# Kernel tuning notes

Measured on AMD Instinct MI355X. Metric: run time of the kernel, lower is better.

The kernel has to match this reference:

```python
import jax, jax.numpy as jnp
import numpy as np

N_NODES = 50000
N_EDGES = 1600000
IN_DIM = 6
H = 64


def _sage_conv(x, src, dst, W_l, b_l, W_r, num_nodes):
    """PyG SAGEConv (aggr='mean'): out = lin_l(mean_{j in N(i)} x_j) + lin_r(x_i).
    lin_l has bias, lin_r has no bias (PyG default)."""
    # mean-aggregate neighbor features at destination nodes
    agg = jax.ops.segment_sum(x[src], dst, num_segments=num_nodes)          # [N, d]
    cnt = jax.ops.segment_sum(jnp.ones((src.shape[0],), x.dtype), dst,
                              num_segments=num_nodes)                        # [N]
    mean = agg / jnp.maximum(cnt, 1.0)[:, None]
    return mean @ W_l + b_l + x @ W_r


def setup_inputs() -> dict:
    key = jax.random.key(0)
    ks = jax.random.split(key, 8)
    x = jax.random.normal(ks[0], (N_NODES, IN_DIM), dtype=jnp.float32)
    edge_index = jax.random.randint(ks[1], (2, N_EDGES), 0, N_NODES, dtype=jnp.int64)
    # Kaiming-ish scaled params
    def lin(k, fan_in, fan_out):
        return jax.random.normal(k, (fan_in, fan_out), dtype=jnp.float32) / np.sqrt(fan_in)
    return {
        "x": x,
        "edge_index": edge_index,
        "W1_l": lin(ks[2], IN_DIM, H),
        "b1_l": jnp.zeros((H,), jnp.float32),
        "W1_r": lin(ks[3], IN_DIM, H),
        "W2_l": lin(ks[4], H, H),
        "b2_l": jnp.zeros((H,), jnp.float32),
        "W2_r": lin(ks[5], H, H),
    }


def reference(x, edge_index, W1_l, b1_l, W1_r, W2_l, b2_l, W2_r):
    src, dst = edge_index[0], edge_index[1]
    n = x.shape[0]
    z = jax.nn.relu(_sage_conv(x, src, dst, W1_l, b1_l, W1_r, n))  # [N, H]
    z = _sage_conv(z, src, dst, W2_l, b2_l, W2_r, n)               # [N, H]
    return z
```

## Files before the change

### kernel.cpp

```cpp
#include <hip/hip_runtime.h>

#define N_NODES 50000
#define N_EDGES 1600000
#define IN_DIM 6
#define H 64

#define NBUCKET 196
#define NBLK 196
#define EPB 8192
#define BCAP 9216

#define L2PAD 72

__device__ __forceinline__ float bf2f(unsigned short u) {
    return __uint_as_float(((unsigned int)u) << 16);
}
__device__ __forceinline__ unsigned short f2bf(float f) {
    unsigned int u = __float_as_uint(f);
    u += 0x7fffu + ((u >> 16) & 1u);
    return (unsigned short)(u >> 16);
}

__global__ __launch_bounds__(512) void scatter_bucketed(
        const int* __restrict__ ei,
        int* __restrict__ gcur,
        unsigned int* __restrict__ ebin,
        const float* __restrict__ W2l,
        const float* __restrict__ W2r,
        unsigned short* __restrict__ Wlt,
        unsigned short* __restrict__ Wrt,
        unsigned short* __restrict__ z) {
    int t = threadIdx.x;
    if (blockIdx.x == NBLK) {
        for (int i = t; i < H * H; i += 512) {
            int k = i >> 6, f = i & 63;
            Wlt[f * H + k] = f2bf(W2l[i]);
            Wrt[f * H + k] = f2bf(W2r[i]);
        }
        if (t < H) z[(size_t)N_NODES * H + t] = 0;
        return;
    }
    __shared__ unsigned int sedge[EPB];
    __shared__ int hist[NBUCKET];
    __shared__ int cur[NBUCKET];
    for (int i = t; i < NBUCKET; i += 512) hist[i] = 0;
    __syncthreads();
    int e0 = blockIdx.x * EPB;
    int cnt = min(EPB, N_EDGES - e0);
    const int4* s4 = (const int4*)(ei + e0);
    const int4* d4 = (const int4*)(ei + N_EDGES + e0);
    for (int k = t; k * 4 < cnt; k += 512) {
        int4 sv = s4[k];
        int4 dv = d4[k];
        sedge[k * 4 + 0] = ((unsigned)sv.x << 16) | (unsigned)dv.x;
        sedge[k * 4 + 1] = ((unsigned)sv.y << 16) | (unsigned)dv.y;
        sedge[k * 4 + 2] = ((unsigned)sv.z << 16) | (unsigned)dv.z;
        sedge[k * 4 + 3] = ((unsigned)sv.w << 16) | (unsigned)dv.w;
        atomicAdd(&hist[dv.x >> 8], 1);
        atomicAdd(&hist[dv.y >> 8], 1);
        atomicAdd(&hist[dv.z >> 8], 1);
        atomicAdd(&hist[dv.w >> 8], 1);
    }
    __syncthreads();
    for (int i = t; i < NBUCKET; i += 512)
        cur[i] = atomicAdd(&gcur[i], hist[i]);
    __syncthreads();
    for (int k = t; k * 4 < cnt; k += 512) {
#pragma unroll
        for (int j = 0; j < 4; j++) {
            unsigned int p = sedge[k * 4 + j];
            int b = (int)(p & 0xffffu) >> 8;
            int pos = atomicAdd(&cur[b], 1);
            if (pos < BCAP) ebin[(size_t)b * BCAP + pos] = p;
        }
    }
}

__global__ __launch_bounds__(1024) void bucket_layer1(
        const unsigned int* __restrict__ ebin,
        const int* __restrict__ gcur,
        const float* __restrict__ x,
        const float* __restrict__ W1l,
        const float* __restrict__ b1,
        const float* __restrict__ W1r,
        int2* __restrict__ rowpair,
        unsigned short* __restrict__ esrc,
        unsigned short* __restrict__ z) {
    __shared__ int raw[BCAP];
    __shared__ unsigned short ssrc[BCAP];
    __shared__ int sdeg[256];
    __shared__ int sstart[256];
    __shared__ int scur[256];
    __shared__ int wsum[4];
    __shared__ float sW1l[IN_DIM * H];
    __shared__ float sW1r[IN_DIM * H];
    float* smx   = (float*)raw;
    float* spart = (float*)raw + 4096;

    int t = threadIdx.x;
    int lane = t & 63, w = t >> 6;
    int b = blockIdx.x;
    int base = b << 8;
    int nn = min(256, N_NODES - base);
    int ebase = b * BCAP;
    int cnt = min(gcur[b], BCAP);

    if (t < 256) sdeg[t] = 0;
    if (t < IN_DIM * H) { sW1l[t] = W1l[t]; sW1r[t] = W1r[t]; }
    for (int i = t; i < cnt; i += 1024) raw[i] = (int)ebin[ebase + i];
    __syncthreads();
    for (int i = t; i < cnt; i += 1024) atomicAdd(&sdeg[raw[i] & 0xff], 1);
    __syncthreads();
    int v = 0, s = 0;
    if (t < 256) {
        v = sdeg[t]; s = v;
#pragma unroll
        for (int off = 1; off < 64; off <<= 1) {
            int u = __shfl_up(s, off);
            if (lane >= off) s += u;
        }
        if (lane == 63) wsum[w] = s;
    }
    __syncthreads();
    if (t < 256) {
        int woff = 0;
        for (int k = 0; k < w; k++) woff += wsum[k];
        int excl = s - v + woff;
        sstart[t] = excl;
        scur[t] = excl;
        if (t < nn) rowpair[base + t] = make_int2(ebase + excl, ebase + excl + v);
    }
    __syncthreads();
    for (int i = t; i < cnt; i += 1024) {
        int p = raw[i];
        int pos = atomicAdd(&scur[p & 0xff], 1);
        ssrc[pos] = (unsigned short)((unsigned)p >> 16);
    }
    __syncthreads();
    for (int i = t; i < cnt; i += 1024)
        esrc[ebase + i] = ssrc[i];
    for (int i = t; i < nn * IN_DIM; i += 1024) {
        int node = i / 6, k = i - node * 6;
        smx[node * 16 + 6 + k] = x[(size_t)base * IN_DIM + i];
    }

    int node = t & 255, q = t >> 8;
    float a0 = 0.f, a1 = 0.f, a2 = 0.f, a3 = 0.f, a4 = 0.f, a5 = 0.f;
    int deg = 0, st = 0;
    if (node < nn) { deg = sdeg[node]; st = sstart[node]; }
    for (int i = st + q; i < st + deg; i += 4) {
        int src = ssrc[i];
        const float2* xs = (const float2*)(x + (size_t)src * IN_DIM);
        float2 p0 = xs[0], p1 = xs[1], p2 = xs[2];
        a0 += p0.x; a1 += p0.y; a2 += p1.x;
        a3 += p1.y; a4 += p2.x; a5 += p2.y;
    }
    if (q > 0 && node < nn) {
        float* sp = &spart[(q - 1) * (256 * 6) + node * 6];
        sp[0] = a0; sp[1] = a1; sp[2] = a2; sp[3] = a3; sp[4] = a4; sp[5] = a5;
    }
    __syncthreads();
    if (q == 0 && node < nn) {
        float inv = 1.0f / fmaxf((float)deg, 1.0f);
        const float* p1p = &spart[0 * (256 * 6) + node * 6];
        const float* p2p = &spart[1 * (256 * 6) + node * 6];
        const float* p3p = &spart[2 * (256 * 6) + node * 6];
        smx[node * 16 + 0] = (a0 + p1p[0] + p2p[0] + p3p[0]) * inv;
        smx[node * 16 + 1] = (a1 + p1p[1] + p2p[1] + p3p[1]) * inv;
        smx[node * 16 + 2] = (a2 + p1p[2] + p2p[2] + p3p[2]) * inv;
        smx[node * 16 + 3] = (a3 + p1p[3] + p2p[3] + p3p[3]) * inv;
        smx[node * 16 + 4] = (a4 + p1p[4] + p2p[4] + p3p[4]) * inv;
        smx[node * 16 + 5] = (a5 + p1p[5] + p2p[5] + p3p[5]) * inv;
    }
    __syncthreads();

    int feat = t & 63, ng = t >> 6;
    float wl[IN_DIM], wr[IN_DIM];
#pragma unroll
    for (int k = 0; k < IN_DIM; k++) { wl[k] = sW1l[k * H + feat]; wr[k] = sW1r[k * H + feat]; }
    float bias = b1[feat];
    for (int nb = ng; nb < nn; nb += 16) {
        const float4* row = (const float4*)&smx[nb * 16];
        float4 r0 = row[0], r1 = row[1], r2 = row[2];
        float acc = bias;
        acc += r0.x * wl[0] + r0.y * wl[1] + r0.z * wl[2]
             + r0.w * wl[3] + r1.x * wl[4] + r1.y * wl[5];
        acc += r1.z * wr[0] + r1.w * wr[1] + r2.x * wr[2]
             + r2.y * wr[3] + r2.z * wr[4] + r2.w * wr[5];
        z[(size_t)(base + nb) * H + feat] = f2bf(fmaxf(acc, 0.0f));
    }
}

__global__ __launch_bounds__(512) void layer2_mfma(
        const unsigned short* __restrict__ zin,
        const int2* __restrict__ rowpair,
        const unsigned short* __restrict__ esrc,
        const unsigned short* __restrict__ Wlt,
        const float* __restrict__ b2,
        const unsigned short* __restrict__ Wrt,
        float* __restrict__ out) {
    typedef short bf16x8 __attribute__((ext_vector_type(8)));
    typedef float f32x4 __attribute__((ext_vector_type(4)));
    __shared__ __attribute__((aligned(16))) unsigned short smean[32 * L2PAD];
    __shared__ __attribute__((aligned(16))) unsigned short szl[32 * L2PAD];
    __shared__ __attribute__((aligned(16))) unsigned short sWl[64 * L2PAD];
    __shared__ __attribute__((aligned(16))) unsigned short sWr[64 * L2PAD];

    int t = threadIdx.x;
    int w = t >> 6, lane = t & 63;
    int g = lane >> 4, lg = lane & 15;
    int n0 = blockIdx.x * 32;

    {
        const ushort4* wl4 = (const ushort4*)Wlt;
        const ushort4* wr4 = (const ushort4*)Wrt;
        for (int qi = t; qi < H * H / 4; qi += 512) {
            int f = qi >> 4, kq = qi & 15;
            *(ushort4*)&sWl[f * L2PAD + kq * 4] = wl4[qi];
            *(ushort4*)&sWr[f * L2PAD + kq * 4] = wr4[qi];
        }
    }

    for (int q = 0; q < 4; q++) {
        int ln = w * 4 + q;
        int n = n0 + ln;
        bool valid = (n < N_NODES);
        int r0 = 0, r1 = 0;
        if (valid) { int2 rp = rowpair[n]; r0 = rp.x; r1 = rp.y; }
        float4 acc = make_float4(0.f, 0.f, 0.f, 0.f);
        for (int base = r0; base < r1; base += 64) {
            int ii = base + lane;
            int idx = (ii < r1) ? (int)esrc[ii] : N_NODES;
            int rem = r1 - base;
#pragma unroll 1
            for (int c = 0; c < 64; c += 16) {
                if (c >= rem) break;
#pragma unroll
                for (int tt = 0; tt < 4; tt++) {
                    int j = c + tt * 4 + g;
                    int s = __shfl(idx, j);
                    const ushort4* zr = (const ushort4*)(zin + (size_t)s * H);
                    ushort4 vv = zr[lg];
                    acc.x += bf2f(vv.x); acc.y += bf2f(vv.y);
                    acc.z += bf2f(vv.z); acc.w += bf2f(vv.w);
                }
            }
        }
#pragma unroll
        for (int off = 16; off < 64; off <<= 1) {
            acc.x += __shfl_xor(acc.x, off);
            acc.y += __shfl_xor(acc.y, off);
            acc.z += __shfl_xor(acc.z, off);
            acc.w += __shfl_xor(acc.w, off);
        }
        float inv = 1.0f / fmaxf((float)(r1 - r0), 1.0f);
        if (g == 0) {
            ushort4 mb;
            mb.x = f2bf(acc.x * inv); mb.y = f2bf(acc.y * inv);
            mb.z = f2bf(acc.z * inv); mb.w = f2bf(acc.w * inv);
            *(ushort4*)&smean[ln * L2PAD + lg * 4] = mb;
        }
        int nz = valid ? n : N_NODES;
        szl[ln * L2PAD + lane] = zin[(size_t)nz * H + lane];
    }
    __syncthreads();

    int nb = w >> 2, fb = w & 3;
    f32x4 acc = {0.f, 0.f, 0.f, 0.f};
#pragma unroll
    for (int ks = 0; ks < 2; ks++) {
        int ko = ks * 32 + g * 8;
        bf16x8 aM = *(const bf16x8*)&smean[(nb * 16 + lg) * L2PAD + ko];
        bf16x8 aZ = *(const bf16x8*)&szl[(nb * 16 + lg) * L2PAD + ko];
        bf16x8 bL = *(const bf16x8*)&sWl[(fb * 16 + lg) * L2PAD + ko];
        bf16x8 bR = *(const bf16x8*)&sWr[(fb * 16 + lg) * L2PAD + ko];
        acc = __builtin_amdgcn_mfma_f32_16x16x32_bf16(aM, bL, acc, 0, 0, 0);
        acc = __builtin_amdgcn_mfma_f32_16x16x32_bf16(aZ, bR, acc, 0, 0, 0);
    }
    float bias = b2[fb * 16 + lg];
#pragma unroll
    for (int r = 0; r < 4; r++) {
        int node = n0 + nb * 16 + g * 4 + r;
        if (node < N_NODES)
            out[(size_t)node * H + fb * 16 + lg] = acc[r] + bias;
    }
}

extern "C" void kernel_launch(void* const* d_in, const int* in_sizes, int n_in,
                              void* d_out, int out_size, void* d_ws, size_t ws_size,
                              hipStream_t stream) {
    const float* x   = (const float*)d_in[0];
    const int*   ei  = (const int*)d_in[1];
    const float* W1l = (const float*)d_in[2];
    const float* b1  = (const float*)d_in[3];
    const float* W1r = (const float*)d_in[4];
    const float* W2l = (const float*)d_in[5];
    const float* b2  = (const float*)d_in[6];
    const float* W2r = (const float*)d_in[7];
    float* out = (float*)d_out;

    int* gcur = (int*)d_ws;
    int2* rowpair = (int2*)(gcur + 208);
    unsigned int*   ebin = (unsigned int*)(rowpair + N_NODES);
    unsigned short* esrc = (unsigned short*)(ebin + (size_t)NBUCKET * BCAP);
    unsigned short* z    = esrc + (size_t)NBUCKET * BCAP;
    unsigned short* Wlt  = z + (size_t)(N_NODES + 1) * H;
    unsigned short* Wrt  = Wlt + H * H;

    hipMemsetAsync(gcur, 0, NBUCKET * sizeof(int), stream);

    scatter_bucketed<<<NBLK + 1, 512, 0, stream>>>(ei, gcur, ebin,
                                                   W2l, W2r, Wlt, Wrt, z);
    bucket_layer1<<<NBUCKET, 1024, 0, stream>>>(ebin, gcur, x, W1l, b1, W1r,
                                                rowpair, esrc, z);
    layer2_mfma<<<(N_NODES + 31) / 32, 512, 0, stream>>>(z, rowpair, esrc,
                                                         Wlt, b2, Wrt, out);
}
```

Before: 150.3 us.

## Fuse three SAGE kernels into one cooperative persistent kernel with grid syncs

Replaces the three separate kernels (edge bucketing, layer-1 aggregation, layer-2 MFMA) with a single cooperative kernel of 256 blocks of 1024 threads, separated by grid-wide syncs. This removes two kernel launch boundaries. Layer 2 becomes a persistent loop over 64-node tiles, and the W2 bf16 transpose now happens in shared memory in every block. x is also repacked into a padded 8-float row so the neighbour gather can use float4 loads. The trade-offs are grid-sync cost, lower occupancy for the layer-2 phase with only 256 blocks, and register pressure from a single 1024-thread launch bound.

Result: slower. 247.8 us (+64.8%).

```diff
diff --git a/kernel.cpp b/kernel.cpp
--- a/kernel.cpp
+++ b/kernel.cpp
@@ -1,4 +1,7 @@
 #include <hip/hip_runtime.h>
+#include <hip/hip_cooperative_groups.h>
+
+namespace cg = cooperative_groups;
 
 #define N_NODES 50000
 #define N_EDGES 1600000
@@ -9,8 +12,12 @@
 #define NBLK 196
 #define EPB 8192
 #define BCAP 9216
-
 #define L2PAD 72
+#define GRID 256
+#define NT ((N_NODES + 63) / 64)
+
+typedef short bf16x8 __attribute__((ext_vector_type(8)));
+typedef float f32x4 __attribute__((ext_vector_type(4)));
 
 __device__ __forceinline__ float bf2f(unsigned short u) {
     return __uint_as_float(((unsigned int)u) << 16);
@@ -21,268 +28,261 @@
     return (unsigned short)(u >> 16);
 }
 
-__global__ __launch_bounds__(512) void scatter_bucketed(
+__global__ __launch_bounds__(1024) void fused_sage(
+        const float* __restrict__ x,
         const int* __restrict__ ei,
-        int* __restrict__ gcur,
-        unsigned int* __restrict__ ebin,
-        const float* __restrict__ W2l,
-        const float* __restrict__ W2r,
-        unsigned short* __restrict__ Wlt,
-        unsigned short* __restrict__ Wrt,
-        unsigned short* __restrict__ z) {
-    int t = threadIdx.x;
-    if (blockIdx.x == NBLK) {
-        for (int i = t; i < H * H; i += 512) {
-            int k = i >> 6, f = i & 63;
-            Wlt[f * H + k] = f2bf(W2l[i]);
-            Wrt[f * H + k] = f2bf(W2r[i]);
-        }
-        if (t < H) z[(size_t)N_NODES * H + t] = 0;
-        return;
-    }
-    __shared__ unsigned int sedge[EPB];
-    __shared__ int hist[NBUCKET];
-    __shared__ int cur[NBUCKET];
-    for (int i = t; i < NBUCKET; i += 512) hist[i] = 0;
-    __syncthreads();
-    int e0 = blockIdx.x * EPB;
-    int cnt = min(EPB, N_EDGES - e0);
-    const int4* s4 = (const int4*)(ei + e0);
-    const int4* d4 = (const int4*)(ei + N_EDGES + e0);
-    for (int k = t; k * 4 < cnt; k += 512) {
-        int4 sv = s4[k];
-        int4 dv = d4[k];
-        sedge[k * 4 + 0] = ((unsigned)sv.x << 16) | (unsigned)dv.x;
-        sedge[k * 4 + 1] = ((unsigned)sv.y << 16) | (unsigned)dv.y;
-        sedge[k * 4 + 2] = ((unsigned)sv.z << 16) | (unsigned)dv.z;
-        sedge[k * 4 + 3] = ((unsigned)sv.w << 16) | (unsigned)dv.w;
-        atomicAdd(&hist[dv.x >> 8], 1);
-        atomicAdd(&hist[dv.y >> 8], 1);
-        atomicAdd(&hist[dv.z >> 8], 1);
-        atomicAdd(&hist[dv.w >> 8], 1);
-    }
-    __syncthreads();
-    for (int i = t; i < NBUCKET; i += 512)
-        cur[i] = atomicAdd(&gcur[i], hist[i]);
-    __syncthreads();
-    for (int k = t; k * 4 < cnt; k += 512) {
-#pragma unroll
-        for (int j = 0; j < 4; j++) {
-            unsigned int p = sedge[k * 4 + j];
-            int b = (int)(p & 0xffffu) >> 8;
-            int pos = atomicAdd(&cur[b], 1);
-            if (pos < BCAP) ebin[(size_t)b * BCAP + pos] = p;
-        }
-    }
-}
-
-__global__ __launch_bounds__(1024) void bucket_layer1(
-        const unsigned int* __restrict__ ebin,
-        const int* __restrict__ gcur,
-        const float* __restrict__ x,
         const float* __restrict__ W1l,
         const float* __restrict__ b1,
         const float* __restrict__ W1r,
+        const float* __restrict__ W2l,
+        const float* __restrict__ b2,
+        const float* __restrict__ W2r,
+        int* __restrict__ gcur,
         int2* __restrict__ rowpair,
+        unsigned int* __restrict__ ebin,
         unsigned short* __restrict__ esrc,
-        unsigned short* __restrict__ z) {
-    __shared__ int raw[BCAP];
-    __shared__ unsigned short ssrc[BCAP];
-    __shared__ int sdeg[256];
-    __shared__ int sstart[256];
-    __shared__ int scur[256];
-    __shared__ int wsum[4];
-    __shared__ float sW1l[IN_DIM * H];
-    __shared__ float sW1r[IN_DIM * H];
-    float* smx   = (float*)raw;
-    float* spart = (float*)raw + 4096;
-
+        unsigned short* __restrict__ z,
+        float* __restrict__ xp,
+        float* __restrict__ out) {
+    __shared__ __attribute__((aligned(16))) unsigned char smem[61456];
     int t = threadIdx.x;
-    int lane = t & 63, w = t >> 6;
-    int b = blockIdx.x;
-    int base = b << 8;
-    int nn = min(256, N_NODES - base);
-    int ebase = b * BCAP;
-    int cnt = min(gcur[b], BCAP);
-
-    if (t < 256) sdeg[t] = 0;
-    if (t < IN_DIM * H) { sW1l[t] = W1l[t]; sW1r[t] = W1r[t]; }
-    for (int i = t; i < cnt; i += 1024) raw[i] = (int)ebin[ebase + i];
-    __syncthreads();
-    for (int i = t; i < cnt; i += 1024) atomicAdd(&sdeg[raw[i] & 0xff], 1);
-    __syncthreads();
-    int v = 0, s = 0;
-    if (t < 256) {
-        v = sdeg[t]; s = v;
-#pragma unroll
-        for (int off = 1; off < 64; off <<= 1) {
-            int u = __shfl_up(s, off);
-            if (lane >= off) s += u;
-        }
-        if (lane == 63) wsum[w] = s;
+    int blk = blockIdx.x;
+    cg::grid_group gg = cg::this_grid();
+
+    {
+        int gid = blk * 1024 + t;
+        if (gid < N_NODES) {
+            const float2* xr = (const float2*)(x + (size_t)gid * IN_DIM);
+            float2 p0 = xr[0], p1 = xr[1], p2 = xr[2];
+            float4* xw = (float4*)(xp + ((size_t)gid << 3));
+            xw[0] = make_float4(p0.x, p0.y, p1.x, p1.y);
+            xw[1] = make_float4(p2.x, p2.y, 0.f, 0.f);
+        }
+        if (blk == NBLK && t < H) z[(size_t)N_NODES * H + t] = 0;
+
+        if (blk < NBLK) {
+            unsigned int* sedge = (unsigned int*)smem;
+            int* hist = (int*)(smem + 32768);
+            int* cur  = (int*)(smem + 33568);
+            if (t < NBUCKET) hist[t] = 0;
+            __syncthreads();
+            int e0 = blk * EPB;
+            int cnt = min(EPB, N_EDGES - e0);
+            const int4* s4 = (const int4*)(ei + e0);
+            const int4* d4 = (const int4*)(ei + N_EDGES + e0);
+            for (int k = t; k * 4 < cnt; k += 1024) {
+                int4 sv = s4[k];
+                int4 dv = d4[k];
+                sedge[k * 4 + 0] = ((unsigned)sv.x << 16) | (unsigned)dv.x;
+                sedge[k * 4 + 1] = ((unsigned)sv.y << 16) | (unsigned)dv.y;
+                sedge[k * 4 + 2] = ((unsigned)sv.z << 16) | (unsigned)dv.z;
+                sedge[k * 4 + 3] = ((unsigned)sv.w << 16) | (unsigned)dv.w;
+                atomicAdd(&hist[dv.x >> 8], 1);
+                atomicAdd(&hist[dv.y >> 8], 1);
+                atomicAdd(&hist[dv.z >> 8], 1);
+                atomicAdd(&hist[dv.w >> 8], 1);
+            }
+            __syncthreads();
+            if (t < NBUCKET) cur[t] = atomicAdd(&gcur[t], hist[t]);
+            __syncthreads();
+            for (int k = t; k * 4 < cnt; k += 1024) {
+#pragma unroll
+                for (int j = 0; j < 4; j++) {
+                    unsigned int p = sedge[k * 4 + j];
+                    int b = (int)(p & 0xffffu) >> 8;
+                    int pos = atomicAdd(&cur[b], 1);
+                    if (pos < BCAP) ebin[(size_t)b * BCAP + pos] = p;
+                }
+            }
+        }
     }
-    __syncthreads();
-    if (t < 256) {
-        int woff = 0;
-        for (int k = 0; k < w; k++) woff += wsum[k];
-        int excl = s - v + woff;
-        sstart[t] = excl;
-        scur[t] = excl;
-        if (t < nn) rowpair[base + t] = make_int2(ebase + excl, ebase + excl + v);
+    gg.sync();
+
+    if (blk < NBUCKET) {
+        int* raw = (int*)smem;
+        unsigned short* ssrc = (unsigned short*)(smem + 36864);
+        int* sdeg   = (int*)(smem + 55296);
+        int* sstart = (int*)(smem + 56320);
+        int* scur   = (int*)(smem + 57344);
+        int* wsum   = (int*)(smem + 58368);
+        float* sW1l = (float*)(smem + 58384);
+        float* sW1r = (float*)(smem + 59920);
+        float* smx   = (float*)smem;
+        float* spart = (float*)smem + 4096;
+
+        int lane = t & 63, w = t >> 6;
+        int base = blk << 8;
+        int nn = min(256, N_NODES - base);
+        int ebase = blk * BCAP;
+        int cnt = min(gcur[blk], BCAP);
+
+        if (t < 256) sdeg[t] = 0;
+        if (t < IN_DIM * H) { sW1l[t] = W1l[t]; sW1r[t] = W1r[t]; }
+        for (int i = t; i < cnt; i += 1024) raw[i] = (int)ebin[ebase + i];
+        __syncthreads();
+        for (int i = t; i < cnt; i += 1024) atomicAdd(&sdeg[raw[i] & 0xff], 1);
+        __syncthreads();
+        int v = 0, s = 0;
+        if (t < 256) {
+            v = sdeg[t]; s = v;
+#pragma unroll
+            for (int off = 1; off < 64; off <<= 1) {
+                int u = __shfl_up(s, off);
+                if (lane >= off) s += u;
+            }
+            if (lane == 63) wsum[w] = s;
+        }
+        __syncthreads();
+        if (t < 256) {
+            int woff = 0;
+            for (int k = 0; k < w; k++) woff += wsum[k];
+            int excl = s - v + woff;
+            sstart[t] = excl;
+            scur[t] = excl;
+            if (t < nn) rowpair[base + t] = make_int2(ebase + excl, ebase + excl + v);
+        }
+        __syncthreads();
+        for (int i = t; i < cnt; i += 1024) {
+            int p = raw[i];
+            int pos = atomicAdd(&scur[p & 0xff], 1);
+            ssrc[pos] = (unsigned short)((unsigned)p >> 16);
+        }
+        __syncthreads();
+        for (int i = t; i < cnt; i += 1024)
+            esrc[ebase + i] = ssrc[i];
+        for (int i = t; i < nn * 8; i += 1024) {
+            int node = i >> 3, k = i & 7;
+            if (k < 6) smx[node * 16 + 6 + k] = xp[(size_t)(base + node) * 8 + k];
+        }
+
+        int node = t & 255, q = t >> 8;
+        float a0 = 0.f, a1 = 0.f, a2 = 0.f, a3 = 0.f, a4 = 0.f, a5 = 0.f;
+        int deg = 0, st = 0;
+        if (node < nn) { deg = sdeg[node]; st = sstart[node]; }
+        for (int i = st + q; i < st + deg; i += 4) {
+            int src = ssrc[i];
+            const float4* xs = (const float4*)(xp + ((size_t)src << 3));
+            float4 p0 = xs[0], p1 = xs[1];
+            a0 += p0.x; a1 += p0.y; a2 += p0.z;
+            a3 += p0.w; a4 += p1.x; a5 += p1.y;
+        }
+        if (q > 0 && node < nn) {
+            float* sp = &spart[(q - 1) * (256 * 6) + node * 6];
+            sp[0] = a0; sp[1] = a1; sp[2] = a2; sp[3] = a3; sp[4] = a4; sp[5] = a5;
+        }
+        __syncthreads();
+        if (q == 0 && node < nn) {
+            float inv = 1.0f / fmaxf((float)deg, 1.0f);
+            const float* p1p = &spart[0 * (256 * 6) + node * 6];
+            const float* p2p = &spart[1 * (256 * 6) + node * 6];
+            const float* p3p = &spart[2 * (256 * 6) + node * 6];
+            smx[node * 16 + 0] = (a0 + p1p[0] + p2p[0] + p3p[0]) * inv;
+            smx[node * 16 + 1] = (a1 + p1p[1] + p2p[1] + p3p[1]) * inv;
+            smx[node * 16 + 2] = (a2 + p1p[2] + p2p[2] + p3p[2]) * inv;
+            smx[node * 16 + 3] = (a3 + p1p[3] + p2p[3] + p3p[3]) * inv;
+            smx[node * 16 + 4] = (a4 + p1p[4] + p2p[4] + p3p[4]) * inv;
+            smx[node * 16 + 5] = (a5 + p1p[5] + p2p[5] + p3p[5]) * inv;
+        }
+        __syncthreads();
+
+        int feat = t & 63, ng = t >> 6;
+        float wl[IN_DIM], wr[IN_DIM];
+#pragma unroll
+        for (int k = 0; k < IN_DIM; k++) { wl[k] = sW1l[k * H + feat]; wr[k] = sW1r[k * H + feat]; }
+        float bias = b1[feat];
+        for (int nb = ng; nb < nn; nb += 16) {
+            const float4* row = (const float4*)&smx[nb * 16];
+            float4 r0 = row[0], r1 = row[1], r2 = row[2];
+            float acc = bias;
+            acc += r0.x * wl[0] + r0.y * wl[1] + r0.z * wl[2]
+                 + r0.w * wl[3] + r1.x * wl[4] + r1.y * wl[5];
+            acc += r1.z * wr[0] + r1.w * wr[1] + r2.x * wr[2]
+                 + r2.y * wr[3] + r2.z * wr[4] + r2.w * wr[5];
+            z[(size_t)(base + nb) * H + feat] = f2bf(fmaxf(acc, 0.0f));
+        }
     }
-    __syncthreads();
-    for (int i = t; i < cnt; i += 1024) {
-        int p = raw[i];
-        int pos = atomicAdd(&scur[p & 0xff], 1);
-        ssrc[pos] = (unsigned short)((unsigned)p >> 16);
-    }
-    __syncthreads();
-    for (int i = t; i < cnt; i += 1024)
-        esrc[ebase + i] = ssrc[i];
-    for (int i = t; i < nn * IN_DIM; i += 1024) {
-        int node = i / 6, k = i - node * 6;
-        smx[node * 16 + 6 + k] = x[(size_t)base * IN_DIM + i];
-    }
-
-    int node = t & 255, q = t >> 8;
-    float a0 = 0.f, a1 = 0.f, a2 = 0.f, a3 = 0.f, a4 = 0.f, a5 = 0.f;
-    int deg = 0, st = 0;
-    if (node < nn) { deg = sdeg[node]; st = sstart[node]; }
-    for (int i = st + q; i < st + deg; i += 4) {
-        int src = ssrc[i];
-        const float2* xs = (const float2*)(x + (size_t)src * IN_DIM);
-        float2 p0 = xs[0], p1 = xs[1], p2 = xs[2];
-        a0 += p0.x; a1 += p0.y; a2 += p1.x;
-        a3 += p1.y; a4 += p2.x; a5 += p2.y;
-    }
-    if (q > 0 && node < nn) {
-        float* sp = &spart[(q - 1) * (256 * 6) + node * 6];
-        sp[0] = a0; sp[1] = a1; sp[2] = a2; sp[3] = a3; sp[4] = a4; sp[5] = a5;
-    }
-    __syncthreads();
-    if (q == 0 && node < nn) {
-        float inv = 1.0f / fmaxf((float)deg, 1.0f);
-        const float* p1p = &spart[0 * (256 * 6) + node * 6];
-        const float* p2p = &spart[1 * (256 * 6) + node * 6];
-        const float* p3p = &spart[2 * (256 * 6) + node * 6];
-        smx[node * 16 + 0] = (a0 + p1p[0] + p2p[0] + p3p[0]) * inv;
-        smx[node * 16 + 1] = (a1 + p1p[1] + p2p[1] + p3p[1]) * inv;
-        smx[node * 16 + 2] = (a2 + p1p[2] + p2p[2] + p3p[2]) * inv;
-        smx[node * 16 + 3] = (a3 + p1p[3] + p2p[3] + p3p[3]) * inv;
-        smx[node * 16 + 4] = (a4 + p1p[4] + p2p[4] + p3p[4]) * inv;
-        smx[node * 16 + 5] = (a5 + p1p[5] + p2p[5] + p3p[5]) * inv;
-    }
-    __syncthreads();
-
-    int feat = t & 63, ng = t >> 6;
-    float wl[IN_DIM], wr[IN_DIM];
-#pragma unroll
-    for (int k = 0; k < IN_DIM; k++) { wl[k] = sW1l[k * H + feat]; wr[k] = sW1r[k * H + feat]; }
-    float bias = b1[feat];
-    for (int nb = ng; nb < nn; nb += 16) {
-        const float4* row = (const float4*)&smx[nb * 16];
-        float4 r0 = row[0], r1 = row[1], r2 = row[2];
-        float acc = bias;
-        acc += r0.x * wl[0] + r0.y * wl[1] + r0.z * wl[2]
-             + r0.w * wl[3] + r1.x * wl[4] + r1.y * wl[5];
-        acc += r1.z * wr[0] + r1.w * wr[1] + r2.x * wr[2]
-             + r2.y * wr[3] + r2.z * wr[4] + r2.w * wr[5];
-        z[(size_t)(base + nb) * H + feat] = f2bf(fmaxf(acc, 0.0f));
-    }
-}
-
-__global__ __launch_bounds__(512) void layer2_mfma(
-        const unsigned short* __restrict__ zin,
-        const int2* __restrict__ rowpair,
-        const unsigned short* __restrict__ esrc,
-        const unsigned short* __restrict__ Wlt,
-        const float* __restrict__ b2,
-        const unsigned short* __restrict__ Wrt,
-        float* __restrict__ out) {
-    typedef short bf16x8 __attribute__((ext_vector_type(8)));
-    typedef float f32x4 __attribute__((ext_vector_type(4)));
-    __shared__ __attribute__((aligned(16))) unsigned short smean[32 * L2PAD];
-    __shared__ __attribute__((aligned(16))) unsigned short szl[32 * L2PAD];
-    __shared__ __attribute__((aligned(16))) unsigned short sWl[64 * L2PAD];
-    __shared__ __attribute__((aligned(16))) unsigned short sWr[64 * L2PAD];
-
-    int t = threadIdx.x;
-    int w = t >> 6, lane = t & 63;
-    int g = lane >> 4, lg = lane & 15;
-    int n0 = blockIdx.x * 32;
+    gg.sync();
 
     {
-        const ushort4* wl4 = (const ushort4*)Wlt;
-        const ushort4* wr4 = (const ushort4*)Wrt;
-        for (int qi = t; qi < H * H / 4; qi += 512) {
-            int f = qi >> 4, kq = qi & 15;
-            *(ushort4*)&sWl[f * L2PAD + kq * 4] = wl4[qi];
-            *(ushort4*)&sWr[f * L2PAD + kq * 4] = wr4[qi];
-        }
-    }
-
-    for (int q = 0; q < 4; q++) {
-        int ln = w * 4 + q;
-        int n = n0 + ln;
-        bool valid = (n < N_NODES);
-        int r0 = 0, r1 = 0;
-        if (valid) { int2 rp = rowpair[n]; r0 = rp.x; r1 = rp.y; }
-        float4 acc = make_float4(0.f, 0.f, 0.f, 0.f);
-        for (int base = r0; base < r1; base += 64) {
-            int ii = base + lane;
-            int idx = (ii < r1) ? (int)esrc[ii] : N_NODES;
-            int rem = r1 - base;
+        unsigned short* smean = (unsigned short*)smem;
+        unsigned short* szl   = (unsigned short*)(smem + 9216);
+        unsigned short* sWl   = (unsigned short*)(smem + 18432);
+        unsigned short* sWr   = (unsigned short*)(smem + 27648);
+
+        for (int i = t; i < H * H; i += 1024) {
+            int k = i >> 6, f = i & 63;
+            sWl[f * L2PAD + k] = f2bf(W2l[i]);
+            sWr[f * L2PAD + k] = f2bf(W2r[i]);
+        }
+        int w = t >> 6, lane = t & 63;
+        int g = lane >> 4, lg = lane & 15;
+        int nb = w >> 2, fb = w & 3;
+        float bias = b2[fb * 16 + lg];
+
+        for (int tile = blk; tile < NT; tile += GRID) {
+            int n0 = tile * 64;
+            for (int q = 0; q < 4; q++) {
+                int ln = w * 4 + q;
+                int n = n0 + ln;
+                bool valid = (n < N_NODES);
+                int r0 = 0, r1 = 0;
+                if (valid) { int2 rp = rowpair[n]; r0 = rp.x; r1 = rp.y; }
+                float4 a = make_float4(0.f, 0.f, 0.f, 0.f);
+                for (int eb = r0; eb < r1; eb += 64) {
+                    int ii = eb + lane;
+                    int idx = (ii < r1) ? (int)esrc[ii] : N_NODES;
+                    int rem = r1 - eb;
 #pragma unroll 1
-            for (int c = 0; c < 64; c += 16) {
-                if (c >= rem) break;
-#pragma unroll
-                for (int tt = 0; tt < 4; tt++) {
-                    int j = c + tt * 4 + g;
-                    int s = __shfl(idx, j);
-                    const ushort4* zr = (const ushort4*)(zin + (size_t)s * H);
-                    ushort4 vv = zr[lg];
-                    acc.x += bf2f(vv.x); acc.y += bf2f(vv.y);
-                    acc.z += bf2f(vv.z); acc.w += bf2f(vv.w);
+                    for (int c = 0; c < 64; c += 16) {
+                        if (c >= rem) break;
+#pragma unroll
+                        for (int tt = 0; tt < 4; tt++) {
+                            int j = c + tt * 4 + g;
+                            int s = __shfl(idx, j);
+                            const ushort4* zr = (const ushort4*)(z + (size_t)s * H);
+                            ushort4 vv = zr[lg];
+                            a.x += bf2f(vv.x); a.y += bf2f(vv.y);
+                            a.z += bf2f(vv.z); a.w += bf2f(vv.w);
+                        }
+                    }
                 }
-            }
-        }
-#pragma unroll
-        for (int off = 16; off < 64; off <<= 1) {
-            acc.x += __shfl_xor(acc.x, off);
-            acc.y += __shfl_xor(acc.y, off);
-            acc.z += __shfl_xor(acc.z, off);
-            acc.w += __shfl_xor(acc.w, off);
-        }
-        float inv = 1.0f / fmaxf((float)(r1 - r0), 1.0f);
-        if (g == 0) {
-            ushort4 mb;
-            mb.x = f2bf(acc.x * inv); mb.y = f2bf(acc.y * inv);
-            mb.z = f2bf(acc.z * inv); mb.w = f2bf(acc.w * inv);
-            *(ushort4*)&smean[ln * L2PAD + lg * 4] = mb;
-        }
-        int nz = valid ? n : N_NODES;
-        szl[ln * L2PAD + lane] = zin[(size_t)nz * H + lane];
-    }
-    __syncthreads();
-
-    int nb = w >> 2, fb = w & 3;
-    f32x4 acc = {0.f, 0.f, 0.f, 0.f};
-#pragma unroll
-    for (int ks = 0; ks < 2; ks++) {
-        int ko = ks * 32 + g * 8;
-        bf16x8 aM = *(const bf16x8*)&smean[(nb * 16 + lg) * L2PAD + ko];
-        bf16x8 aZ = *(const bf16x8*)&szl[(nb * 16 + lg) * L2PAD + ko];
-        bf16x8 bL = *(const bf16x8*)&sWl[(fb * 16 + lg) * L2PAD + ko];
-        bf16x8 bR = *(const bf16x8*)&sWr[(fb * 16 + lg) * L2PAD + ko];
-        acc = __builtin_amdgcn_mfma_f32_16x16x32_bf16(aM, bL, acc, 0, 0, 0);
-        acc = __builtin_amdgcn_mfma_f32_16x16x32_bf16(aZ, bR, acc, 0, 0, 0);
-    }
-    float bias = b2[fb * 16 + lg];
-#pragma unroll
-    for (int r = 0; r < 4; r++) {
-        int node = n0 + nb * 16 + g * 4 + r;
-        if (node < N_NODES)
-            out[(size_t)node * H + fb * 16 + lg] = acc[r] + bias;
+#pragma unroll
+                for (int off = 16; off < 64; off <<= 1) {
+                    a.x += __shfl_xor(a.x, off);
+                    a.y += __shfl_xor(a.y, off);
+                    a.z += __shfl_xor(a.z, off);
+                    a.w += __shfl_xor(a.w, off);
+                }
+                float inv = 1.0f / fmaxf((float)(r1 - r0), 1.0f);
+                if (g == 0) {
+                    ushort4 mb;
+                    mb.x = f2bf(a.x * inv); mb.y = f2bf(a.y * inv);
+                    mb.z = f2bf(a.z * inv); mb.w = f2bf(a.w * inv);
+                    *(ushort4*)&smean[ln * L2PAD + lg * 4] = mb;
+                }
+                int nz = valid ? n : N_NODES;
+                szl[ln * L2PAD + lane] = z[(size_t)nz * H + lane];
+            }
+            __syncthreads();
+            f32x4 acc = {0.f, 0.f, 0.f, 0.f};
+#pragma unroll
+            for (int ks = 0; ks < 2; ks++) {
+                int ko = ks * 32 + g * 8;
+                bf16x8 aM = *(const bf16x8*)&smean[(nb * 16 + lg) * L2PAD + ko];
+                bf16x8 aZ = *(const bf16x8*)&szl[(nb * 16 + lg) * L2PAD + ko];
+                bf16x8 bL = *(const bf16x8*)&sWl[(fb * 16 + lg) * L2PAD + ko];
+                bf16x8 bR = *(const bf16x8*)&sWr[(fb * 16 + lg) * L2PAD + ko];
+                acc = __builtin_amdgcn_mfma_f32_16x16x32_bf16(aM, bL, acc, 0, 0, 0);
+                acc = __builtin_amdgcn_mfma_f32_16x16x32_bf16(aZ, bR, acc, 0, 0, 0);
+            }
+#pragma unroll
+            for (int r = 0; r < 4; r++) {
+                int node = n0 + nb * 16 + g * 4 + r;
+                if (node < N_NODES)
+                    out[(size_t)node * H + fb * 16 + lg] = acc[r] + bias;
+            }
+            __syncthreads();
+        }
     }
 }
 
@@ -304,15 +304,14 @@
     unsigned int*   ebin = (unsigned int*)(rowpair + N_NODES);
     unsigned short* esrc = (unsigned short*)(ebin + (size_t)NBUCKET * BCAP);
     unsigned short* z    = esrc + (size_t)NBUCKET * BCAP;
-    unsigned short* Wlt  = z + (size_t)(N_NODES + 1) * H;
-    unsigned short* Wrt  = Wlt + H * H;
+    float* xp = (float*)(z + (size_t)(N_NODES + 1) * H);
 
     hipMemsetAsync(gcur, 0, NBUCKET * sizeof(int), stream);
 
-    scatter_bucketed<<<NBLK + 1, 512, 0, stream>>>(ei, gcur, ebin,
-                                                   W2l, W2r, Wlt, Wrt, z);
-    bucket_layer1<<<NBUCKET, 1024, 0, stream>>>(ebin, gcur, x, W1l, b1, W1r,
-                                                rowpair, esrc, z);
-    layer2_mfma<<<(N_NODES + 31) / 32, 512, 0, stream>>>(z, rowpair, esrc,
-                                                         Wlt, b2, Wrt, out);
+    void* args[] = {(void*)&x, (void*)&ei, (void*)&W1l, (void*)&b1, (void*)&W1r,
+                    (void*)&W2l, (void*)&b2, (void*)&W2r,
+                    (void*)&gcur, (void*)&rowpair, (void*)&ebin, (void*)&esrc,
+                    (void*)&z, (void*)&xp, (void*)&out};
+    hipLaunchCooperativeKernel((void*)fused_sage, dim3(GRID), dim3(1024),
+                               args, 0, stream);
 }
```
